# Kernel tuning notes

Hardware: AMD Instinct MI355X
Metric: run time of the kernel (lower is better)

## Reference

```python
import jax, jax.numpy as jnp
import numpy as np

B, S, D_IN = 2, 2048, 2048
HEADS, HEAD_DIM, N_KV = 32, 64, 8
GROUP = HEADS // N_KV
EPS = 1e-6


def setup_inputs() -> dict:
    key = jax.random.key(0)
    ks = jax.random.split(key, 8)
    x = jax.random.normal(ks[0], (B, S, D_IN), dtype=jnp.float32)
    # causal additive mask: 0 on/below diagonal, -inf above
    mask = jnp.where(jnp.tril(jnp.ones((S, S), dtype=bool)), 0.0, -jnp.inf).astype(jnp.float32)
    # standard RoPE tables over half-dim, tiled to head_dim (rotate-half convention)
    inv_freq = 1.0 / (10000.0 ** (np.arange(0, HEAD_DIM, 2, dtype=np.float32) / HEAD_DIM))
    angles = np.arange(S, dtype=np.float32)[:, None] * inv_freq[None, :]  # [S, D/2]
    angles = np.concatenate([angles, angles], axis=-1)  # [S, D]
    cos = jnp.asarray(np.cos(angles), dtype=jnp.float32)
    sin = jnp.asarray(np.sin(angles), dtype=jnp.float32)
    s = 0.02
    Wq = jax.random.normal(ks[1], (D_IN, HEADS * HEAD_DIM), dtype=jnp.float32) * s
    Wk = jax.random.normal(ks[2], (D_IN, N_KV * HEAD_DIM), dtype=jnp.float32) * s
    Wv = jax.random.normal(ks[3], (D_IN, N_KV * HEAD_DIM), dtype=jnp.float32) * s
    Wo = jax.random.normal(ks[4], (HEADS * HEAD_DIM, D_IN), dtype=jnp.float32) * s
    q_scale = jnp.ones((HEAD_DIM,), dtype=jnp.float32)
    k_scale = jnp.ones((HEAD_DIM,), dtype=jnp.float32)
    return {"x": x, "mask": mask, "cos": cos, "sin": sin,
            "Wq": Wq, "Wk": Wk, "Wv": Wv, "Wo": Wo,
            "q_scale": q_scale, "k_scale": k_scale}


def _rmsnorm(t, w):
    # Qwen3-style RMSNorm over head_dim (computed in fp32)
    var = jnp.mean(jnp.square(t), axis=-1, keepdims=True)
    return (t * jax.lax.rsqrt(var + EPS)) * w


def _rotate_half(t):
    h = t.shape[-1] // 2
    return jnp.concatenate([-t[..., h:], t[..., :h]], axis=-1)


def _rope(t, cos, sin):
    # t: [B, H, S, D]; cos/sin: [S, D]
    return t * cos[None, None, :, :] + _rotate_half(t) * sin[None, None, :, :]


def reference(x, mask, cos, sin, Wq, Wk, Wv, Wo, q_scale, k_scale):
    Bsz, seq, _ = x.shape
    Q = (x @ Wq).reshape(Bsz, seq, HEADS, HEAD_DIM).transpose(0, 2, 1, 3)  # [B,H,S,D]
    K = (x @ Wk).reshape(Bsz, seq, N_KV, HEAD_DIM).transpose(0, 2, 1, 3)   # [B,G,S,D]
    V = (x @ Wv).reshape(Bsz, seq, N_KV, HEAD_DIM).transpose(0, 2, 1, 3)   # [B,G,S,D]
    Q = _rmsnorm(Q, q_scale)
    K = _rmsnorm(K, k_scale)
    Q = _rope(Q, cos[:seq], sin[:seq])
    K = _rope(K, cos[:seq], sin[:seq])
    K = jnp.repeat(K, GROUP, axis=1)  # [B,H,S,D]
    V = jnp.repeat(V, GROUP, axis=1)
    scores = jnp.einsum('bhqd,bhkd->bhqk', Q, K) + mask[:seq, :seq]
    weights = jax.nn.softmax(scores / jnp.sqrt(jnp.float32(HEAD_DIM)), axis=-1)
    vectors = jnp.einsum('bhqk,bhkd->bhqd', weights, V)
    vectors = vectors.transpose(0, 2, 1, 3).reshape(Bsz, seq, HEADS * HEAD_DIM)
    return vectors @ Wo
```

## Files before the change

### kernel.cpp

```cpp
#include <hip/hip_runtime.h>
#include <hip/hip_bf16.h>
#include <stdint.h>

#define S_LEN   2048
#define DIN     2048
#define NHEADS  32
#define HDIM    64
#define NKV     8

typedef __bf16 bf16x8 __attribute__((ext_vector_type(8)));
typedef float  f32x4  __attribute__((ext_vector_type(4)));

#define AS1(p) ((__attribute__((address_space(1))) void*)(void*)(p))
#define AS3(p) ((__attribute__((address_space(3))) void*)(p))
#define MFMA_BF16 __builtin_amdgcn_mfma_f32_16x16x32_bf16

#if __has_builtin(__builtin_amdgcn_exp2f)
#define EXP2F(x) __builtin_amdgcn_exp2f(x)
#else
#define EXP2F(x) exp2f(x)
#endif

static __device__ __forceinline__ unsigned short f2bf(float f) {
  unsigned int x = __float_as_uint(f);
  return (unsigned short)((x + 0x7fffu + ((x >> 16) & 1u)) >> 16);
}
static __device__ __forceinline__ float bf2f(unsigned short u) {
  return __uint_as_float((unsigned int)u << 16);
}

__global__ __launch_bounds__(256) void prep_kernel(const float* __restrict__ x,
                                                   const float* __restrict__ Wq,
                                                   const float* __restrict__ Wk,
                                                   const float* __restrict__ Wv,
                                                   const float* __restrict__ Wo,
                                                   unsigned short* __restrict__ xb,
                                                   unsigned short* __restrict__ wcat,
                                                   unsigned short* __restrict__ wo_t) {
  const int bid = blockIdx.x;
  if (bid < 8192) {
    int i = bid * 256 + threadIdx.x;
    float4 f = ((const float4*)x)[i];
    ((ushort4*)xb)[i] = make_ushort4(f2bf(f.x), f2bf(f.y), f2bf(f.z), f2bf(f.w));
    return;
  }
  __shared__ float t[32][33];
  const int tx = threadIdx.x & 31, ty = threadIdx.x >> 5;
  const float* src; unsigned short* dst; int n0, k0, col0, srcN, dstK;
  if (bid < 14336) {
    int b2 = bid - 8192;
    n0 = (b2 % 96) * 32; k0 = (b2 / 96) * 32;
    if (n0 < 2048)      { src = Wq; col0 = n0;        srcN = 2048; }
    else if (n0 < 2560) { src = Wk; col0 = n0 - 2048; srcN = 512; }
    else                { src = Wv; col0 = n0 - 2560; srcN = 512; }
    dst = wcat; dstK = 2048;
  } else {
    int b3 = bid - 14336;
    n0 = (b3 % 64) * 32; k0 = (b3 / 64) * 32;
    src = Wo; col0 = n0; srcN = 2048; dst = wo_t; dstK = 2048;
  }
  #pragma unroll
  for (int j = 0; j < 32; j += 8)
    t[ty + j][tx] = src[(size_t)(k0 + ty + j) * srcN + col0 + tx];
  __syncthreads();
  #pragma unroll
  for (int j = 0; j < 32; j += 8)
    dst[(size_t)(n0 + ty + j) * dstK + k0 + tx] = f2bf(t[tx][ty + j]);
}

template <typename OutT>
__global__ __launch_bounds__(256) void gemm_nt(const unsigned short* __restrict__ A,
                                               const unsigned short* __restrict__ Bt,
                                               OutT* __restrict__ C,
                                               int M, int N, int K) {
  __shared__ alignas(16) unsigned short As[2][4096];
  __shared__ alignas(16) unsigned short Bs[2][4096];
  const int tid = threadIdx.x;
  const int wave = tid >> 6, lane = tid & 63;
  const int g = lane >> 4, c = lane & 15;
  const int m0 = blockIdx.y * 128, n0 = blockIdx.x * 128;
  const int wm = (wave & 1) * 64, wn = (wave >> 1) * 64;

  f32x4 acc[4][4] = {};

  const int ch0 = wave * 2;
  const int p0 = ch0 * 64 + lane, p1 = p0 + 64;
  const int r0 = p0 >> 2, gc0 = ((p0 & 3) ^ ((r0 >> 1) & 3)) * 8;
  const int r1 = p1 >> 2, gc1 = ((p1 & 3) ^ ((r1 >> 1) & 3)) * 8;
  const unsigned short* a0 = A + (size_t)(m0 + r0) * K + gc0;
  const unsigned short* a1 = A + (size_t)(m0 + r1) * K + gc1;
  const unsigned short* b0 = Bt + (size_t)(n0 + r0) * K + gc0;
  const unsigned short* b1 = Bt + (size_t)(n0 + r1) * K + gc1;
  const int fswz = (c >> 1) & 3;

  for (int k0 = 0; k0 < K; k0 += 64) {
    __syncthreads();
    __builtin_amdgcn_global_load_lds(AS1(a0 + k0), AS3(&As[0][ch0 * 512]), 16, 0, 0);
    __builtin_amdgcn_global_load_lds(AS1(a1 + k0), AS3(&As[0][ch0 * 512 + 512]), 16, 0, 0);
    __builtin_amdgcn_global_load_lds(AS1(b0 + k0), AS3(&Bs[0][ch0 * 512]), 16, 0, 0);
    __builtin_amdgcn_global_load_lds(AS1(b1 + k0), AS3(&Bs[0][ch0 * 512 + 512]), 16, 0, 0);
    __builtin_amdgcn_global_load_lds(AS1(a0 + k0 + 32), AS3(&As[1][ch0 * 512]), 16, 0, 0);
    __builtin_amdgcn_global_load_lds(AS1(a1 + k0 + 32), AS3(&As[1][ch0 * 512 + 512]), 16, 0, 0);
    __builtin_amdgcn_global_load_lds(AS1(b0 + k0 + 32), AS3(&Bs[1][ch0 * 512]), 16, 0, 0);
    __builtin_amdgcn_global_load_lds(AS1(b1 + k0 + 32), AS3(&Bs[1][ch0 * 512 + 512]), 16, 0, 0);
    __builtin_amdgcn_s_waitcnt(0);
    __syncthreads();

    #pragma unroll
    for (int h = 0; h < 2; h++) {
      bf16x8 af[4], bfr[4];
      #pragma unroll
      for (int i = 0; i < 4; i++)
        af[i] = *(const bf16x8*)(&As[h][(wm + i * 16 + c) * 32 + (g ^ fswz) * 8]);
      #pragma unroll
      for (int j = 0; j < 4; j++)
        bfr[j] = *(const bf16x8*)(&Bs[h][(wn + j * 16 + c) * 32 + (g ^ fswz) * 8]);
      #pragma unroll
      for (int i = 0; i < 4; i++)
        #pragma unroll
        for (int j = 0; j < 4; j++)
          acc[i][j] = MFMA_BF16(af[i], bfr[j], acc[i][j], 0, 0, 0);
    }
  }

  #pragma unroll
  for (int i = 0; i < 4; i++)
    #pragma unroll
    for (int j = 0; j < 4; j++)
      #pragma unroll
      for (int r = 0; r < 4; r++) {
        size_t idx = (size_t)(m0 + wm + i * 16 + g * 4 + r) * N + n0 + wn + j * 16 + c;
        if constexpr (sizeof(OutT) == 2) C[idx] = f2bf(acc[i][j][r]);
        else                             C[idx] = acc[i][j][r];
      }
}

__global__ __launch_bounds__(256) void norm_rope_vt(const unsigned short* __restrict__ QKV,
                                                    const float* __restrict__ cosb,
                                                    const float* __restrict__ sinb,
                                                    const float* __restrict__ q_scale,
                                                    const float* __restrict__ k_scale,
                                                    unsigned short* __restrict__ Qn,
                                                    unsigned short* __restrict__ Kn,
                                                    unsigned short* __restrict__ Vt) {
  const int tid = threadIdx.x;
  if (blockIdx.x >= 10240) {
    __shared__ unsigned int t[64][65];
    int bid = blockIdx.x - 10240;
    const int st = bid & 31, kv = (bid >> 5) & 7, b = bid >> 8;
    const int lane = tid & 63, quad = tid >> 6;
    #pragma unroll
    for (int p = 0; p < 16; p++) {
      int sl = p * 4 + quad;
      t[sl][lane] = QKV[(size_t)(b * 2048 + st * 64 + sl) * 3072 + 2560 + kv * 64 + lane];
    }
    __syncthreads();
    size_t base = (size_t)(b * 8 + kv) * 64 * 2048;
    #pragma unroll
    for (int p = 0; p < 16; p++) {
      int dd = p * 4 + quad;
      Vt[base + (size_t)dd * 2048 + st * 64 + lane] = (unsigned short)t[lane][dd];
    }
    return;
  }
  const int w = tid >> 6, d = tid & 63;
  const float qs = q_scale[d], ks = k_scale[d];
  #pragma unroll
  for (int k = 0; k < 4; k++) {
    int task = blockIdx.x * 16 + w * 4 + k;
    const int hid = task % 40;
    const int row = task / 40;
    const int b = row >> 11, s = row & 2047;
    float val, sc;
    if (hid < 32) {
      val = bf2f(QKV[(size_t)row * 3072 + hid * 64 + d]);
      sc = qs;
    } else {
      val = bf2f(QKV[(size_t)row * 3072 + 2048 + (hid - 32) * 64 + d]);
      sc = ks;
    }
    float v2 = val * val;
    #pragma unroll
    for (int off = 32; off; off >>= 1) v2 += __shfl_xor(v2, off);
    float t = val * (1.0f / sqrtf(v2 * (1.0f / 64.0f) + 1e-6f)) * sc;
    float partner = __shfl_xor(t, 32);
    float rot = (d < 32) ? -partner : partner;
    float o = t * cosb[s * 64 + d] + rot * sinb[s * 64 + d];
    if (hid < 32) o *= 0.18033688011112042f;
    unsigned short ob = f2bf(o);
    if (hid < 32) Qn[((size_t)(b * 32 + hid) * 2048 + s) * 64 + d] = ob;
    else          Kn[((size_t)(b * 8 + (hid - 32)) * 2048 + s) * 64 + d] = ob;
  }
}

__global__ __launch_bounds__(256, 3) void attn_kernel(const unsigned short* __restrict__ Qn,
                                                      const unsigned short* __restrict__ Kn,
                                                      const unsigned short* __restrict__ Vt,
                                                      unsigned short* __restrict__ Outv) {
  __shared__ alignas(16) unsigned short Ksh[2][4096];
  __shared__ alignas(16) unsigned short Vsh[2][4096];
  __shared__ alignas(16) char Psh[4][4352];

  const int tid = threadIdx.x, w = tid >> 6, lane = tid & 63;
  const int g = lane >> 4, c = lane & 15;
  const int cs = c & 7;
  const int rl = (lane >> 3) & 7;
  const int sl = lane & 7;
  const int swz = (sl ^ rl) << 3;
  const int bid = blockIdx.x;
  const int qt = 63 - (bid >> 4);
  const int rem = bid & 15;
  const int hg = rem & 7, b = rem >> 3;
  const int h = hg * 4 + w;
  const int Q0 = qt * 32;
  const unsigned short* Qp = Qn + ((size_t)(b * NHEADS + h) * S_LEN + Q0) * HDIM;
  const unsigned short* Kp = Kn + (size_t)(b * NKV + hg) * S_LEN * HDIM;
  const unsigned short* Vp = Vt + (size_t)(b * NKV + hg) * HDIM * S_LEN;
  const int ntiles = (qt >> 1) + 1;
  char* PwB = Psh[w];

  bf16x8 bq[2][2];
  #pragma unroll
  for (int iq = 0; iq < 2; iq++)
    #pragma unroll
    for (int t = 0; t < 2; t++)
      bq[iq][t] = *(const bf16x8*)(Qp + (iq * 16 + c) * HDIM + t * 32 + g * 8);

  f32x4 OT[4][2] = {};
  float lv[2] = {0.f, 0.f};

  const int wr0 = w * 16;

  auto STAGE = [&](int kv0s, int bi) {
    #pragma unroll
    for (int q = 0; q < 2; q++) {
      const int rr = wr0 + q * 8;
      __builtin_amdgcn_global_load_lds(AS1(Kp + (size_t)(kv0s + rr + rl) * 64 + swz),
                                       AS3(&Ksh[bi][rr * 64]), 16, 0, 0);
      __builtin_amdgcn_global_load_lds(AS1(Vp + (size_t)(rr + rl) * 2048 + kv0s + swz),
                                       AS3(&Vsh[bi][rr * 64]), 16, 0, 0);
    }
  };

  STAGE(0, 0);
  __syncthreads();

  for (int ti = 0; ti < ntiles; ti++) {
    const int kv0 = ti * 64;
    const int cur = ti & 1;
    if (ti + 1 < ntiles) STAGE(kv0 + 64, cur ^ 1);

    const unsigned short* Kb = Ksh[cur];
    const unsigned short* Vb = Vsh[cur];

    #pragma unroll
    for (int jb = 0; jb < 2; jb++) {
      bf16x8 akx[2][2];
      #pragma unroll
      for (int jt = 0; jt < 2; jt++)
        #pragma unroll
        for (int t = 0; t < 2; t++)
          akx[jt][t] = *(const bf16x8*)(Kb + ((jb * 2 + jt) * 16 + c) * 64 +
                                        (((t * 4 + g) ^ cs) << 3));
      f32x4 Sx[2][2] = {};
      __builtin_amdgcn_s_setprio(1);
      #pragma unroll
      for (int t = 0; t < 2; t++)
        #pragma unroll
        for (int jt = 0; jt < 2; jt++)
          #pragma unroll
          for (int iq = 0; iq < 2; iq++)
            Sx[jt][iq] = MFMA_BF16(akx[jt][t], bq[iq][t], Sx[jt][iq], 0, 0, 0);
      __builtin_amdgcn_s_setprio(0);

      if (ti == ntiles - 1) {
        #pragma unroll
        for (int jt = 0; jt < 2; jt++)
          #pragma unroll
          for (int iq = 0; iq < 2; iq++)
            #pragma unroll
            for (int r = 0; r < 4; r++) {
              int kv = kv0 + (jb * 2 + jt) * 16 + g * 4 + r;
              int q  = Q0 + iq * 16 + c;
              if (kv > q) Sx[jt][iq][r] = -1e30f;
            }
      }

      #pragma unroll
      for (int jt = 0; jt < 2; jt++)
        #pragma unroll
        for (int iq = 0; iq < 2; iq++) {
          f32x4 p;
          #pragma unroll
          for (int r = 0; r < 4; r++) p[r] = EXP2F(Sx[jt][iq][r]);
          lv[iq] += (p[0] + p[1]) + (p[2] + p[3]);
          uint32_t u0 = __float_as_uint(p[0]) + 0x8000u;
          uint32_t u1 = __float_as_uint(p[1]) + 0x8000u;
          uint32_t u2 = __float_as_uint(p[2]) + 0x8000u;
          uint32_t u3 = __float_as_uint(p[3]) + 0x8000u;
          uint32_t lo = __builtin_amdgcn_perm(u1, u0, 0x07060302u);
          uint32_t hi = __builtin_amdgcn_perm(u3, u2, 0x07060302u);
          int row = iq * 16 + c;
          int bytecol = (jb * 2 + jt) * 32 + g * 8;
          uint32_t off = row * 128 + (((bytecol >> 4) ^ (row & 7)) << 4) + (bytecol & 15);
          *(uint2*)(PwB + off) = make_uint2(lo, hi);
        }
    }

    __builtin_amdgcn_s_waitcnt(0xC07F);

    #pragma unroll
    for (int t = 0; t < 2; t++) {
      bf16x8 avt[4];
      #pragma unroll
      for (int dt = 0; dt < 4; dt++)
        avt[dt] = *(const bf16x8*)(Vb + (dt * 16 + c) * 64 + (((t * 4 + g) ^ cs) << 3));
      bf16x8 bpt[2];
      #pragma unroll
      for (int iq = 0; iq < 2; iq++) {
        int row = iq * 16 + c;
        int bytecol = t * 64 + g * 16;
        uint32_t off = row * 128 + (((bytecol >> 4) ^ (row & 7)) << 4);
        bpt[iq] = *(const bf16x8*)(PwB + off);
      }
      __builtin_amdgcn_s_setprio(1);
      #pragma unroll
      for (int dt = 0; dt < 4; dt++)
        #pragma unroll
        for (int iq = 0; iq < 2; iq++)
          OT[dt][iq] = MFMA_BF16(avt[dt], bpt[iq], OT[dt][iq], 0, 0, 0);
      __builtin_amdgcn_s_setprio(0);
    }

    if (ti + 1 < ntiles) __syncthreads();
  }

  float inv[2];
  #pragma unroll
  for (int iq = 0; iq < 2; iq++) {
    float s = lv[iq];
    s += __shfl_xor(s, 16);
    s += __shfl_xor(s, 32);
    inv[iq] = 1.0f / s;
  }

  #pragma unroll
  for (int iq = 0; iq < 2; iq++) {
    const int q = Q0 + iq * 16 + c;
    unsigned short* orow = Outv + (size_t)(b * S_LEN + q) * (NHEADS * HDIM) + h * HDIM;
    #pragma unroll
    for (int dt = 0; dt < 4; dt++) {
      uint32_t u0 = __float_as_uint(OT[dt][iq][0] * inv[iq]) + 0x8000u;
      uint32_t u1 = __float_as_uint(OT[dt][iq][1] * inv[iq]) + 0x8000u;
      uint32_t u2 = __float_as_uint(OT[dt][iq][2] * inv[iq]) + 0x8000u;
      uint32_t u3 = __float_as_uint(OT[dt][iq][3] * inv[iq]) + 0x8000u;
      uint32_t lo = __builtin_amdgcn_perm(u1, u0, 0x07060302u);
      uint32_t hi = __builtin_amdgcn_perm(u3, u2, 0x07060302u);
      *(uint2*)(orow + dt * 16 + g * 4) = make_uint2(lo, hi);
    }
  }
}

extern "C" void kernel_launch(void* const* d_in, const int* in_sizes, int n_in,
                              void* d_out, int out_size, void* d_ws, size_t ws_size,
                              hipStream_t stream) {
  const float* x       = (const float*)d_in[0];
  const float* cosb    = (const float*)d_in[2];
  const float* sinb    = (const float*)d_in[3];
  const float* Wq      = (const float*)d_in[4];
  const float* Wk      = (const float*)d_in[5];
  const float* Wv      = (const float*)d_in[6];
  const float* Wo      = (const float*)d_in[7];
  const float* q_scale = (const float*)d_in[8];
  const float* k_scale = (const float*)d_in[9];

  char* ws = (char*)d_ws;
  unsigned short* xb   = (unsigned short*)(ws);
  unsigned short* wcat = (unsigned short*)(ws + (16ull << 20));
  unsigned short* wo_t = (unsigned short*)(ws + (28ull << 20));
  unsigned short* qkv  = (unsigned short*)(ws + (36ull << 20));
  unsigned short* qn   = (unsigned short*)(ws + (84ull << 20));
  unsigned short* kn   = (unsigned short*)(ws + (100ull << 20));
  unsigned short* vt   = (unsigned short*)(ws + (104ull << 20));
  unsigned short* vec  = (unsigned short*)(ws + (36ull << 20));

  prep_kernel<<<18432, 256, 0, stream>>>(x, Wq, Wk, Wv, Wo, xb, wcat, wo_t);
  gemm_nt<unsigned short><<<dim3(24, 32), 256, 0, stream>>>(xb, wcat, qkv, 4096, 3072, 2048);
  norm_rope_vt<<<10752, 256, 0, stream>>>(qkv, cosb, sinb, q_scale, k_scale, qn, kn, vt);
  attn_kernel<<<1024, 256, 0, stream>>>(qn, kn, vt, vec);
  gemm_nt<float><<<dim3(16, 32), 256, 0, stream>>>(vec, wo_t, (float*)d_out, 4096, 2048, 2048);
}
```

Measured before the change: 315.0 us.

## Process 64-query tiles per attention block and swizzle GEMM blocks across XCDs

The attention kernel now handles two 32-row query subtiles per block, so each staged K/V tile is reused twice and the grid is halved. The P scratch buffer is doubled and launch bounds lowered to 2 blocks per CU to fit the extra accumulators. The GEMMs use a 1D grid remapped so consecutive blocks on the same XCD share tiles, aiming for better L2 locality. The tradeoff is lower occupancy, coarser causal load balance, and some wasted masked work in the diagonal tile.

```diff
diff --git a/kernel.cpp b/kernel.cpp
--- a/kernel.cpp
+++ b/kernel.cpp
@@ -72,13 +72,16 @@
 __global__ __launch_bounds__(256) void gemm_nt(const unsigned short* __restrict__ A,
                                                const unsigned short* __restrict__ Bt,
                                                OutT* __restrict__ C,
-                                               int M, int N, int K) {
+                                               int M, int N, int K, int nxb) {
   __shared__ alignas(16) unsigned short As[2][4096];
   __shared__ alignas(16) unsigned short Bs[2][4096];
   const int tid = threadIdx.x;
   const int wave = tid >> 6, lane = tid & 63;
   const int g = lane >> 4, c = lane & 15;
-  const int m0 = blockIdx.y * 128, n0 = blockIdx.x * 128;
+  const int id = blockIdx.x;
+  const int cpx = gridDim.x >> 3;
+  const int swb = (id & 7) * cpx + (id >> 3);
+  const int m0 = (swb / nxb) * 128, n0 = (swb % nxb) * 128;
   const int wm = (wave & 1) * 64, wn = (wave >> 1) * 64;
 
   f32x4 acc[4][4] = {};
@@ -193,13 +196,13 @@
   }
 }
 
-__global__ __launch_bounds__(256, 3) void attn_kernel(const unsigned short* __restrict__ Qn,
+__global__ __launch_bounds__(256, 2) void attn_kernel(const unsigned short* __restrict__ Qn,
                                                       const unsigned short* __restrict__ Kn,
                                                       const unsigned short* __restrict__ Vt,
                                                       unsigned short* __restrict__ Outv) {
   __shared__ alignas(16) unsigned short Ksh[2][4096];
   __shared__ alignas(16) unsigned short Vsh[2][4096];
-  __shared__ alignas(16) char Psh[4][4352];
+  __shared__ alignas(16) char Psh[4][8704];
 
   const int tid = threadIdx.x, w = tid >> 6, lane = tid & 63;
   const int g = lane >> 4, c = lane & 15;
@@ -208,26 +211,29 @@
   const int sl = lane & 7;
   const int swz = (sl ^ rl) << 3;
   const int bid = blockIdx.x;
-  const int qt = 63 - (bid >> 4);
+  const int u = 31 - (bid >> 4);
   const int rem = bid & 15;
   const int hg = rem & 7, b = rem >> 3;
   const int h = hg * 4 + w;
-  const int Q0 = qt * 32;
+  const int Q0 = u * 64;
   const unsigned short* Qp = Qn + ((size_t)(b * NHEADS + h) * S_LEN + Q0) * HDIM;
   const unsigned short* Kp = Kn + (size_t)(b * NKV + hg) * S_LEN * HDIM;
   const unsigned short* Vp = Vt + (size_t)(b * NKV + hg) * HDIM * S_LEN;
-  const int ntiles = (qt >> 1) + 1;
-  char* PwB = Psh[w];
-
-  bf16x8 bq[2][2];
+  const int ntiles = u + 1;
+  char* PA = Psh[w];
+  char* PB = PA + 4352;
+
+  bf16x8 bqA[2][2], bqB[2][2];
   #pragma unroll
   for (int iq = 0; iq < 2; iq++)
     #pragma unroll
-    for (int t = 0; t < 2; t++)
-      bq[iq][t] = *(const bf16x8*)(Qp + (iq * 16 + c) * HDIM + t * 32 + g * 8);
-
-  f32x4 OT[4][2] = {};
-  float lv[2] = {0.f, 0.f};
+    for (int t = 0; t < 2; t++) {
+      bqA[iq][t] = *(const bf16x8*)(Qp + (iq * 16 + c) * HDIM + t * 32 + g * 8);
+      bqB[iq][t] = *(const bf16x8*)(Qp + (32 + iq * 16 + c) * HDIM + t * 32 + g * 8);
+    }
+
+  f32x4 OTA[4][2] = {}, OTB[4][2] = {};
+  float lvA[2] = {0.f, 0.f}, lvB[2] = {0.f, 0.f};
 
   const int wr0 = w * 16;
 
@@ -254,109 +260,127 @@
     const unsigned short* Vb = Vsh[cur];
 
     #pragma unroll
-    for (int jb = 0; jb < 2; jb++) {
-      bf16x8 akx[2][2];
-      #pragma unroll
-      for (int jt = 0; jt < 2; jt++)
-        #pragma unroll
-        for (int t = 0; t < 2; t++)
-          akx[jt][t] = *(const bf16x8*)(Kb + ((jb * 2 + jt) * 16 + c) * 64 +
-                                        (((t * 4 + g) ^ cs) << 3));
-      f32x4 Sx[2][2] = {};
-      __builtin_amdgcn_s_setprio(1);
-      #pragma unroll
-      for (int t = 0; t < 2; t++)
+    for (int qtile = 0; qtile < 2; qtile++) {
+      const int qbase = Q0 + qtile * 32;
+      char* Pw = qtile ? PB : PA;
+      #pragma unroll
+      for (int jb = 0; jb < 2; jb++) {
+        bf16x8 akx[2][2];
         #pragma unroll
         for (int jt = 0; jt < 2; jt++)
           #pragma unroll
-          for (int iq = 0; iq < 2; iq++)
-            Sx[jt][iq] = MFMA_BF16(akx[jt][t], bq[iq][t], Sx[jt][iq], 0, 0, 0);
-      __builtin_amdgcn_s_setprio(0);
-
-      if (ti == ntiles - 1) {
+          for (int t = 0; t < 2; t++)
+            akx[jt][t] = *(const bf16x8*)(Kb + ((jb * 2 + jt) * 16 + c) * 64 +
+                                          (((t * 4 + g) ^ cs) << 3));
+        f32x4 Sx[2][2] = {};
+        __builtin_amdgcn_s_setprio(1);
+        #pragma unroll
+        for (int t = 0; t < 2; t++)
+          #pragma unroll
+          for (int jt = 0; jt < 2; jt++)
+            #pragma unroll
+            for (int iq = 0; iq < 2; iq++)
+              Sx[jt][iq] = MFMA_BF16(akx[jt][t], qtile ? bqB[iq][t] : bqA[iq][t],
+                                     Sx[jt][iq], 0, 0, 0);
+        __builtin_amdgcn_s_setprio(0);
+
+        if (ti == ntiles - 1) {
+          #pragma unroll
+          for (int jt = 0; jt < 2; jt++)
+            #pragma unroll
+            for (int iq = 0; iq < 2; iq++)
+              #pragma unroll
+              for (int r = 0; r < 4; r++) {
+                int kv = kv0 + (jb * 2 + jt) * 16 + g * 4 + r;
+                int q  = qbase + iq * 16 + c;
+                if (kv > q) Sx[jt][iq][r] = -1e30f;
+              }
+        }
+
         #pragma unroll
         for (int jt = 0; jt < 2; jt++)
           #pragma unroll
-          for (int iq = 0; iq < 2; iq++)
+          for (int iq = 0; iq < 2; iq++) {
+            f32x4 p;
             #pragma unroll
-            for (int r = 0; r < 4; r++) {
-              int kv = kv0 + (jb * 2 + jt) * 16 + g * 4 + r;
-              int q  = Q0 + iq * 16 + c;
-              if (kv > q) Sx[jt][iq][r] = -1e30f;
-            }
+            for (int r = 0; r < 4; r++) p[r] = EXP2F(Sx[jt][iq][r]);
+            float ps = (p[0] + p[1]) + (p[2] + p[3]);
+            if (qtile) lvB[iq] += ps; else lvA[iq] += ps;
+            uint32_t u0 = __float_as_uint(p[0]) + 0x8000u;
+            uint32_t u1 = __float_as_uint(p[1]) + 0x8000u;
+            uint32_t u2 = __float_as_uint(p[2]) + 0x8000u;
+            uint32_t u3 = __float_as_uint(p[3]) + 0x8000u;
+            uint32_t lo = __builtin_amdgcn_perm(u1, u0, 0x07060302u);
+            uint32_t hi = __builtin_amdgcn_perm(u3, u2, 0x07060302u);
+            int row = iq * 16 + c;
+            int bytecol = (jb * 2 + jt) * 32 + g * 8;
+            uint32_t off = row * 128 + (((bytecol >> 4) ^ (row & 7)) << 4) + (bytecol & 15);
+            *(uint2*)(Pw + off) = make_uint2(lo, hi);
+          }
       }
 
-      #pragma unroll
-      for (int jt = 0; jt < 2; jt++)
+      __builtin_amdgcn_s_waitcnt(0xC07F);
+
+      #pragma unroll
+      for (int t = 0; t < 2; t++) {
+        bf16x8 avt[4];
+        #pragma unroll
+        for (int dt = 0; dt < 4; dt++)
+          avt[dt] = *(const bf16x8*)(Vb + (dt * 16 + c) * 64 + (((t * 4 + g) ^ cs) << 3));
+        bf16x8 bpt[2];
         #pragma unroll
         for (int iq = 0; iq < 2; iq++) {
-          f32x4 p;
+          int row = iq * 16 + c;
+          int bytecol = t * 64 + g * 16;
+          uint32_t off = row * 128 + (((bytecol >> 4) ^ (row & 7)) << 4);
+          bpt[iq] = *(const bf16x8*)(Pw + off);
+        }
+        __builtin_amdgcn_s_setprio(1);
+        #pragma unroll
+        for (int dt = 0; dt < 4; dt++)
           #pragma unroll
-          for (int r = 0; r < 4; r++) p[r] = EXP2F(Sx[jt][iq][r]);
-          lv[iq] += (p[0] + p[1]) + (p[2] + p[3]);
-          uint32_t u0 = __float_as_uint(p[0]) + 0x8000u;
-          uint32_t u1 = __float_as_uint(p[1]) + 0x8000u;
-          uint32_t u2 = __float_as_uint(p[2]) + 0x8000u;
-          uint32_t u3 = __float_as_uint(p[3]) + 0x8000u;
-          uint32_t lo = __builtin_amdgcn_perm(u1, u0, 0x07060302u);
-          uint32_t hi = __builtin_amdgcn_perm(u3, u2, 0x07060302u);
-          int row = iq * 16 + c;
-          int bytecol = (jb * 2 + jt) * 32 + g * 8;
-          uint32_t off = row * 128 + (((bytecol >> 4) ^ (row & 7)) << 4) + (bytecol & 15);
-          *(uint2*)(PwB + off) = make_uint2(lo, hi);
-        }
-    }
-
-    __builtin_amdgcn_s_waitcnt(0xC07F);
-
-    #pragma unroll
-    for (int t = 0; t < 2; t++) {
-      bf16x8 avt[4];
-      #pragma unroll
-      for (int dt = 0; dt < 4; dt++)
-        avt[dt] = *(const bf16x8*)(Vb + (dt * 16 + c) * 64 + (((t * 4 + g) ^ cs) << 3));
-      bf16x8 bpt[2];
-      #pragma unroll
-      for (int iq = 0; iq < 2; iq++) {
-        int row = iq * 16 + c;
-        int bytecol = t * 64 + g * 16;
-        uint32_t off = row * 128 + (((bytecol >> 4) ^ (row & 7)) << 4);
-        bpt[iq] = *(const bf16x8*)(PwB + off);
+          for (int iq = 0; iq < 2; iq++) {
+            if (qtile) OTB[dt][iq] = MFMA_BF16(avt[dt], bpt[iq], OTB[dt][iq], 0, 0, 0);
+            else       OTA[dt][iq] = MFMA_BF16(avt[dt], bpt[iq], OTA[dt][iq], 0, 0, 0);
+          }
+        __builtin_amdgcn_s_setprio(0);
       }
-      __builtin_amdgcn_s_setprio(1);
-      #pragma unroll
-      for (int dt = 0; dt < 4; dt++)
-        #pragma unroll
-        for (int iq = 0; iq < 2; iq++)
-          OT[dt][iq] = MFMA_BF16(avt[dt], bpt[iq], OT[dt][iq], 0, 0, 0);
-      __builtin_amdgcn_s_setprio(0);
     }
 
     if (ti + 1 < ntiles) __syncthreads();
   }
 
-  float inv[2];
+  float invA[2], invB[2];
   #pragma unroll
   for (int iq = 0; iq < 2; iq++) {
-    float s = lv[iq];
-    s += __shfl_xor(s, 16);
-    s += __shfl_xor(s, 32);
-    inv[iq] = 1.0f / s;
-  }
-
-  #pragma unroll
-  for (int iq = 0; iq < 2; iq++) {
-    const int q = Q0 + iq * 16 + c;
-    unsigned short* orow = Outv + (size_t)(b * S_LEN + q) * (NHEADS * HDIM) + h * HDIM;
-    #pragma unroll
-    for (int dt = 0; dt < 4; dt++) {
-      uint32_t u0 = __float_as_uint(OT[dt][iq][0] * inv[iq]) + 0x8000u;
-      uint32_t u1 = __float_as_uint(OT[dt][iq][1] * inv[iq]) + 0x8000u;
-      uint32_t u2 = __float_as_uint(OT[dt][iq][2] * inv[iq]) + 0x8000u;
-      uint32_t u3 = __float_as_uint(OT[dt][iq][3] * inv[iq]) + 0x8000u;
-      uint32_t lo = __builtin_amdgcn_perm(u1, u0, 0x07060302u);
-      uint32_t hi = __builtin_amdgcn_perm(u3, u2, 0x07060302u);
-      *(uint2*)(orow + dt * 16 + g * 4) = make_uint2(lo, hi);
+    float sA = lvA[iq];
+    sA += __shfl_xor(sA, 16);
+    sA += __shfl_xor(sA, 32);
+    invA[iq] = 1.0f / sA;
+    float sB = lvB[iq];
+    sB += __shfl_xor(sB, 16);
+    sB += __shfl_xor(sB, 32);
+    invB[iq] = 1.0f / sB;
+  }
+
+  #pragma unroll
+  for (int qtile = 0; qtile < 2; qtile++) {
+    #pragma unroll
+    for (int iq = 0; iq < 2; iq++) {
+      const int q = Q0 + qtile * 32 + iq * 16 + c;
+      const float iv = qtile ? invB[iq] : invA[iq];
+      unsigned short* orow = Outv + (size_t)(b * S_LEN + q) * (NHEADS * HDIM) + h * HDIM;
+      #pragma unroll
+      for (int dt = 0; dt < 4; dt++) {
+        const f32x4& o = qtile ? OTB[dt][iq] : OTA[dt][iq];
+        uint32_t u0 = __float_as_uint(o[0] * iv) + 0x8000u;
+        uint32_t u1 = __float_as_uint(o[1] * iv) + 0x8000u;
+        uint32_t u2 = __float_as_uint(o[2] * iv) + 0x8000u;
+        uint32_t u3 = __float_as_uint(o[3] * iv) + 0x8000u;
+        uint32_t lo = __builtin_amdgcn_perm(u1, u0, 0x07060302u);
+        uint32_t hi = __builtin_amdgcn_perm(u3, u2, 0x07060302u);
+        *(uint2*)(orow + dt * 16 + g * 4) = make_uint2(lo, hi);
+      }
     }
   }
 }
@@ -385,8 +409,8 @@
   unsigned short* vec  = (unsigned short*)(ws + (36ull << 20));
 
   prep_kernel<<<18432, 256, 0, stream>>>(x, Wq, Wk, Wv, Wo, xb, wcat, wo_t);
-  gemm_nt<unsigned short><<<dim3(24, 32), 256, 0, stream>>>(xb, wcat, qkv, 4096, 3072, 2048);
+  gemm_nt<unsigned short><<<768, 256, 0, stream>>>(xb, wcat, qkv, 4096, 3072, 2048, 24);
   norm_rope_vt<<<10752, 256, 0, stream>>>(qkv, cosb, sinb, q_scale, k_scale, qn, kn, vt);
-  attn_kernel<<<1024, 256, 0, stream>>>(qn, kn, vt, vec);
-  gemm_nt<float><<<dim3(16, 32), 256, 0, stream>>>(vec, wo_t, (float*)d_out, 4096, 2048, 2048);
-}
+  attn_kernel<<<512, 256, 0, stream>>>(qn, kn, vt, vec);
+  gemm_nt<float><<<512, 256, 0, stream>>>(vec, wo_t, (float*)d_out, 4096, 2048, 2048, 16);
+}
```

Result: slower. 335.5 us (+6.5%).
